# Performance work log

Measured on AMD Instinct MI355X. Metric: run time of the kernel, lower is better.

## Reference

```python
import jax, jax.numpy as jnp
import numpy as np

B, S, D, H = 2, 2048, 1024, 16
HD = D // H

def setup_inputs() -> dict:
    key = jax.random.key(0)
    ks = jax.random.split(key, 9)
    s = 1.0 / np.sqrt(D)
    return {
        "x": jax.random.normal(ks[0], (B, S, D), jnp.float32),
        "Wq": jax.random.normal(ks[1], (D, D), jnp.float32) * s,
        "bq": jnp.zeros((D,), jnp.float32),
        "Wk": jax.random.normal(ks[2], (D, D), jnp.float32) * s,
        "bk": jnp.zeros((D,), jnp.float32),
        "Wv": jax.random.normal(ks[3], (D, D), jnp.float32) * s,
        "bv": jnp.zeros((D,), jnp.float32),
        "Wo": jax.random.normal(ks[4], (D, D), jnp.float32) * s,
        "bo": jnp.zeros((D,), jnp.float32),
    }

def reference(x, Wq, bq, Wk, bk, Wv, bv, Wo, bo):
    b, s, d = x.shape
    def split_heads(t):
        return t.reshape(b, s, H, HD).transpose(0, 2, 1, 3)  # [B,H,S,HD]
    q = split_heads(x @ Wq + bq)
    k = split_heads(x @ Wk + bk)
    v = split_heads(x @ Wv + bv)
    scores = jnp.einsum('bhqd,bhkd->bhqk', q, k) / jnp.sqrt(jnp.float32(HD))
    causal = jnp.tril(jnp.ones((s, s), bool))  # True = keep
    scores = jnp.where(causal, scores, -jnp.inf)
    attn = jax.nn.softmax(scores, axis=-1)
    out = jnp.einsum('bhqk,bhkd->bhqd', attn, v)  # [B,H,S,HD]
    out = out.transpose(0, 2, 1, 3).reshape(b, s, d)
    return out @ Wo + bo
```

## Files before the change

### kernel.cpp

```cpp
#include <hip/hip_runtime.h>

typedef unsigned short u16;
typedef unsigned int u32;
typedef __attribute__((ext_vector_type(8))) short bf16x8;
typedef __attribute__((ext_vector_type(4))) float f32x4;

#define BB 2
#define SS 2048
#define DD 1024
#define HH 16
#define HD 64
#define MM (BB * SS)

__device__ inline float u2f(u32 u) { return __uint_as_float(u); }
__device__ inline u16 f2bf(float f) {
  u32 u = __float_as_uint(f);
  return (u16)((u + 0x7fffu + ((u >> 16) & 1u)) >> 16);
}

__device__ inline int sw(int r, int ci) { return r * 64 + (((ci ^ (r & 7)) & 7) << 3); }

typedef const __attribute__((address_space(1))) void* gas_ptr;
typedef __attribute__((address_space(3))) void* las_ptr;
__device__ __forceinline__ void gll16(const void* g, void* l) {
  __builtin_amdgcn_global_load_lds((gas_ptr)g, (las_ptr)l, 16, 0, 0);
}

__global__ __launch_bounds__(256) void prep(const float* __restrict__ x, u16* __restrict__ xb,
                                            const float* __restrict__ W0, const float* __restrict__ W1,
                                            const float* __restrict__ W2, const float* __restrict__ W3,
                                            u16* __restrict__ Wt) {
  int z = blockIdx.z;
  int t = threadIdx.x;
  if (z >= 4) {
    int gid = (z - 4) * 256 + blockIdx.y * 16 + blockIdx.x;
    int i = (gid * 256 + t) * 8;
    float4 a = *(const float4*)(x + i);
    float4 b = *(const float4*)(x + i + 4);
    uint4 o;
    o.x = (u32)f2bf(a.x) | ((u32)f2bf(a.y) << 16);
    o.y = (u32)f2bf(a.z) | ((u32)f2bf(a.w) << 16);
    o.z = (u32)f2bf(b.x) | ((u32)f2bf(b.y) << 16);
    o.w = (u32)f2bf(b.z) | ((u32)f2bf(b.w) << 16);
    *(uint4*)(xb + i) = o;
    return;
  }
  const float* W = (z == 0) ? W0 : (z == 1) ? W1 : (z == 2) ? W2 : W3;
  u16* out = Wt + (size_t)z * (DD * DD);
  __shared__ __align__(16) u16 T[64][72];
  int n0 = blockIdx.x * 64, k0 = blockIdx.y * 64;
#pragma unroll
  for (int p = 0; p < 4; ++p) {
    int kr = (t >> 4) + p * 16;
    int c4 = (t & 15) * 4;
    float4 v = *(const float4*)&W[(size_t)(k0 + kr) * DD + n0 + c4];
    T[c4 + 0][kr] = f2bf(v.x);
    T[c4 + 1][kr] = f2bf(v.y);
    T[c4 + 2][kr] = f2bf(v.z);
    T[c4 + 3][kr] = f2bf(v.w);
  }
  __syncthreads();
#pragma unroll
  for (int p = 0; p < 2; ++p) {
    int n = (t >> 3) + p * 32;
    int c8 = (t & 7) * 8;
    uint4 v = *(const uint4*)&T[n][c8];
    *(uint4*)&out[(size_t)(n0 + n) * DD + k0 + c8] = v;
  }
}

__global__ __launch_bounds__(256, 3) void gemm_qkv(const u16* __restrict__ xb, const u16* __restrict__ Wt,
                                                   const float* __restrict__ bq, const float* __restrict__ bk,
                                                   const float* __restrict__ bv,
                                                   u16* __restrict__ Qb, u16* __restrict__ Kb, u16* __restrict__ Vtb) {
  __shared__ __align__(16) u16 As[2][128 * 32];
  __shared__ __align__(16) u16 Bs[2][128 * 32];
  const int tid = threadIdx.x, lane = tid & 63, wv = tid >> 6;
  const int wm = (wv >> 1) * 64, wn = (wv & 1) * 64;
  const int l16 = lane & 15, quad = lane >> 4;

  const int id = blockIdx.x;
  const int xcd = id & 7, inner = id >> 3;
  const int mg = xcd >> 1, ng = xcd & 1;
  const int im = inner & 7, rest = inner >> 3;
  const int in_ = rest & 3, z = rest >> 2;
  const int m0 = (mg * 8 + im) * 128, n0 = (ng * 4 + in_) * 128;

  const u16* Bt = Wt + (size_t)z * (DD * DD);
  const float* bias = (z == 0) ? bq : (z == 1) ? bk : bv;

  const int r0 = tid >> 2, k8 = (tid & 3) << 3;
  const u16* Ap0 = &xb[(size_t)(m0 + r0) * DD + k8];
  const u16* Ap1 = Ap0 + (size_t)64 * DD;
  const u16* Bp0 = &Bt[(size_t)(n0 + r0) * DD + k8];
  const u16* Bp1 = Bp0 + (size_t)64 * DD;

  gll16(Ap0, &As[0][wv * 512]);
  gll16(Ap1, &As[0][2048 + wv * 512]);
  gll16(Bp0, &Bs[0][wv * 512]);
  gll16(Bp1, &Bs[0][2048 + wv * 512]);

  f32x4 acc[4][4];
  f32x4 zero = {0.f, 0.f, 0.f, 0.f};
#pragma unroll
  for (int i = 0; i < 4; ++i)
#pragma unroll
    for (int j = 0; j < 4; ++j) acc[i][j] = zero;

  __syncthreads();

  for (int kk = 0; kk < 32; ++kk) {
    const int cur = kk & 1;
    if (kk + 1 < 32) {
      const int nxt = cur ^ 1;
      const int ko = (kk + 1) * 32;
      gll16(Ap0 + ko, &As[nxt][wv * 512]);
      gll16(Ap1 + ko, &As[nxt][2048 + wv * 512]);
      gll16(Bp0 + ko, &Bs[nxt][wv * 512]);
      gll16(Bp1 + ko, &Bs[nxt][2048 + wv * 512]);
    }
    bf16x8 af[4], bg[4];
#pragma unroll
    for (int i = 0; i < 4; ++i) {
      af[i] = *(const bf16x8*)&As[cur][(wm + i * 16 + l16) * 32 + quad * 8];
      bg[i] = *(const bf16x8*)&Bs[cur][(wn + i * 16 + l16) * 32 + quad * 8];
    }
#pragma unroll
    for (int i = 0; i < 4; ++i)
#pragma unroll
      for (int j = 0; j < 4; ++j)
        acc[i][j] = __builtin_amdgcn_mfma_f32_16x16x32_bf16(af[i], bg[j], acc[i][j], 0, 0, 0);
    __syncthreads();
  }

  const float qsc = (z == 0) ? 0.180336880f : 1.0f;
  if (z == 2) {
#pragma unroll
    for (int i = 0; i < 4; ++i) {
#pragma unroll
      for (int j = 0; j < 4; ++j) {
        int col = n0 + wn + j * 16 + l16;
        float bcol = bias[col];
        int hh = col >> 6, dd = col & 63;
        int row0 = m0 + wm + i * 16 + quad * 4;
        int bb = row0 >> 11, s0 = row0 & (SS - 1);
        int sbase = (s0 & ~63) + 16 * quad + ((s0 >> 4) & 3);
        size_t base = (((size_t)((bb * HH + hh) * HD + dd)) << 11) + sbase;
#pragma unroll
        for (int r = 0; r < 4; ++r)
          Vtb[base + 4 * r] = f2bf(acc[i][j][r] + bcol);
      }
    }
  } else {
    u16* out = (z == 0) ? Qb : Kb;
#pragma unroll
    for (int i = 0; i < 4; ++i) {
#pragma unroll
      for (int j = 0; j < 4; ++j) {
        int col = n0 + wn + j * 16 + l16;
        float bcol = bias[col];
        int hh = col >> 6, dd = col & 63;
#pragma unroll
        for (int r = 0; r < 4; ++r) {
          int row = m0 + wm + i * 16 + quad * 4 + r;
          int bb = row >> 11, s = row & (SS - 1);
          out[((size_t)((bb * HH + hh) * SS + s) << 6) | dd] = f2bf((acc[i][j][r] + bcol) * qsc);
        }
      }
    }
  }
}

__global__ __launch_bounds__(256, 3) void gemm_out(const u16* __restrict__ Ub, const u16* __restrict__ Wot,
                                                   const float* __restrict__ bo, float* __restrict__ out) {
  __shared__ __align__(16) u16 As[2][128 * 32];
  __shared__ __align__(16) u16 Bs[2][64 * 32];
  const int tid = threadIdx.x, lane = tid & 63, wv = tid >> 6;
  const int wm = (wv >> 1) * 64, wn = (wv & 1) * 32;
  const int l16 = lane & 15, quad = lane >> 4;
  const int r0 = tid >> 2, k8 = (tid & 3) << 3;

  const int id = blockIdx.x;
  const int xcd = id & 7, inner = id >> 3;
  const int mg = xcd >> 1, ng = xcd & 1;
  const int im = inner & 7, in_ = inner >> 3;
  const int m0 = (mg * 8 + im) * 128, n0 = (ng * 8 + in_) * 64;

  const u16* Ap0 = &Ub[(size_t)(m0 + r0) * DD + k8];
  const u16* Ap1 = Ap0 + (size_t)64 * DD;
  const u16* Bp0 = &Wot[(size_t)(n0 + r0) * DD + k8];

  gll16(Ap0, &As[0][wv * 512]);
  gll16(Ap1, &As[0][2048 + wv * 512]);
  gll16(Bp0, &Bs[0][wv * 512]);

  f32x4 acc[4][2];
  f32x4 zero = {0.f, 0.f, 0.f, 0.f};
#pragma unroll
  for (int i = 0; i < 4; ++i) { acc[i][0] = zero; acc[i][1] = zero; }

  __syncthreads();

  for (int kk = 0; kk < 32; ++kk) {
    const int cur = kk & 1;
    if (kk + 1 < 32) {
      const int nxt = cur ^ 1;
      const int ko = (kk + 1) * 32;
      gll16(Ap0 + ko, &As[nxt][wv * 512]);
      gll16(Ap1 + ko, &As[nxt][2048 + wv * 512]);
      gll16(Bp0 + ko, &Bs[nxt][wv * 512]);
    }
    bf16x8 af[4], bg[2];
#pragma unroll
    for (int i = 0; i < 4; ++i) af[i] = *(const bf16x8*)&As[cur][(wm + i * 16 + l16) * 32 + quad * 8];
#pragma unroll
    for (int j = 0; j < 2; ++j) bg[j] = *(const bf16x8*)&Bs[cur][(wn + j * 16 + l16) * 32 + quad * 8];
#pragma unroll
    for (int i = 0; i < 4; ++i)
#pragma unroll
      for (int j = 0; j < 2; ++j)
        acc[i][j] = __builtin_amdgcn_mfma_f32_16x16x32_bf16(af[i], bg[j], acc[i][j], 0, 0, 0);
    __syncthreads();
  }

#pragma unroll
  for (int i = 0; i < 4; ++i) {
#pragma unroll
    for (int j = 0; j < 2; ++j) {
      int col = n0 + wn + j * 16 + l16;
      float bcol = bo[col];
#pragma unroll
      for (int r = 0; r < 4; ++r) {
        int row = m0 + wm + i * 16 + quad * 4 + r;
        out[(size_t)row * DD + col] = acc[i][j][r] + bcol;
      }
    }
  }
}

__global__ __launch_bounds__(256, 2) void attention_mfma(const u16* __restrict__ Q, const u16* __restrict__ K,
                                                         const u16* __restrict__ Vt, u16* __restrict__ Uo) {
  const int tid = threadIdx.x, lane = tid & 63, wv = tid >> 6;
  const int l16 = lane & 15, quad = lane >> 4;
  const int bh = blockIdx.x & 31;
  const int b = bh >> 4, h = bh & 15;
  const int gq = blockIdx.x >> 5;
  const int qA = (gq < 8) ? gq : 23 - gq;
  const int qB = 31 - qA;
  const int q0A = qA * 64, q0B = qB * 64;
  const u16* Qh = Q + (size_t)(b * HH + h) * SS * HD;
  const u16* Kh = K + (size_t)(b * HH + h) * SS * HD;
  const u16* Vh = Vt + (size_t)(b * HH + h) * HD * SS;

  __shared__ __align__(16) u16 K_lds[2][64 * 64];
  __shared__ __align__(16) u16 V_lds[2][64 * 64];
  __shared__ __align__(16) u16 p_lds[2][64][72];

  bf16x8 qfA0, qfA1, qfB0, qfB1;
  {
    const u16* qa = &Qh[(size_t)(q0A + wv * 16 + l16) * HD + quad * 8];
    qfA0 = *(const bf16x8*)qa;
    qfA1 = *(const bf16x8*)(qa + 32);
    const u16* qb = &Qh[(size_t)(q0B + wv * 16 + l16) * HD + quad * 8];
    qfB0 = *(const bf16x8*)qb;
    qfB1 = *(const bf16x8*)(qb + 32);
  }

  f32x4 zero = {0.f, 0.f, 0.f, 0.f};
  f32x4 oA[4], oB[4];
#pragma unroll
  for (int j = 0; j < 4; ++j) { oA[j] = zero; oB[j] = zero; }
  float lA[4] = {0.f, 0.f, 0.f, 0.f}, lB[4] = {0.f, 0.f, 0.f, 0.f};

  const int sr = tid >> 2, ci = tid & 3, cc = ci << 3;
  const u16* Kg = &Kh[(size_t)sr * HD + cc];
  const u16* Vg = &Vh[(size_t)sr * SS + cc];
  const int ktiles = qB + 1;
  const int wlo = sw(sr, ci), whi = sw(sr, ci + 4);

  uint4 ka = *(const uint4*)Kg, kb = *(const uint4*)(Kg + 32);
  uint4 va = *(const uint4*)Vg, vb = *(const uint4*)(Vg + 32);
  *(uint4*)&K_lds[0][wlo] = ka;
  *(uint4*)&K_lds[0][whi] = kb;
  *(uint4*)&V_lds[0][wlo] = va;
  *(uint4*)&V_lds[0][whi] = vb;
  {
    const u16* Kn = Kg + (size_t)64 * HD;
    const u16* Vn = Vg + 64;
    ka = *(const uint4*)Kn; kb = *(const uint4*)(Kn + 32);
    va = *(const uint4*)Vn; vb = *(const uint4*)(Vn + 32);
  }
  __syncthreads();

  for (int t = 0; t < ktiles; ++t) {
    const int cur = t & 1;
    const bool doA = (t <= qA);

    f32x4 sA[4], sB[4];
#pragma unroll
    for (int n = 0; n < 4; ++n) {
      const int kr = n * 16 + l16;
      bf16x8 kf0 = *(const bf16x8*)&K_lds[cur][sw(kr, quad)];
      bf16x8 kf1 = *(const bf16x8*)&K_lds[cur][sw(kr, quad + 4)];
      f32x4 aB = zero;
      aB = __builtin_amdgcn_mfma_f32_16x16x32_bf16(qfB0, kf0, aB, 0, 0, 0);
      aB = __builtin_amdgcn_mfma_f32_16x16x32_bf16(qfB1, kf1, aB, 0, 0, 0);
      sB[n] = aB;
      if (doA) {
        f32x4 aA = zero;
        aA = __builtin_amdgcn_mfma_f32_16x16x32_bf16(qfA0, kf0, aA, 0, 0, 0);
        aA = __builtin_amdgcn_mfma_f32_16x16x32_bf16(qfA1, kf1, aA, 0, 0, 0);
        sA[n] = aA;
      }
    }

    {
      const int rel = q0B + wv * 16 + quad * 4 - t * 64;
#pragma unroll
      for (int rr = 0; rr < 4; ++rr) {
        float p0 = __builtin_amdgcn_exp2f(sB[0][rr]);
        float p1 = __builtin_amdgcn_exp2f(sB[1][rr]);
        float p2 = __builtin_amdgcn_exp2f(sB[2][rr]);
        float p3 = __builtin_amdgcn_exp2f(sB[3][rr]);
        if (t == qB) {
          int row = rel + rr;
          p0 = (l16 <= row) ? p0 : 0.f;
          p1 = (16 + l16 <= row) ? p1 : 0.f;
          p2 = (32 + l16 <= row) ? p2 : 0.f;
          p3 = (48 + l16 <= row) ? p3 : 0.f;
        }
        lB[rr] += (p0 + p1) + (p2 + p3);
        uint2 pk;
        pk.x = (__float_as_uint(p0) >> 16) | (__float_as_uint(p1) & 0xffff0000u);
        pk.y = (__float_as_uint(p2) >> 16) | (__float_as_uint(p3) & 0xffff0000u);
        *(uint2*)&p_lds[1][wv * 16 + quad * 4 + rr][l16 * 4] = pk;
      }
    }
    if (doA) {
      const int rel = q0A + wv * 16 + quad * 4 - t * 64;
#pragma unroll
      for (int rr = 0; rr < 4; ++rr) {
        float p0 = __builtin_amdgcn_exp2f(sA[0][rr]);
        float p1 = __builtin_amdgcn_exp2f(sA[1][rr]);
        float p2 = __builtin_amdgcn_exp2f(sA[2][rr]);
        float p3 = __builtin_amdgcn_exp2f(sA[3][rr]);
        if (t == qA) {
          int row = rel + rr;
          p0 = (l16 <= row) ? p0 : 0.f;
          p1 = (16 + l16 <= row) ? p1 : 0.f;
          p2 = (32 + l16 <= row) ? p2 : 0.f;
          p3 = (48 + l16 <= row) ? p3 : 0.f;
        }
        lA[rr] += (p0 + p1) + (p2 + p3);
        uint2 pk;
        pk.x = (__float_as_uint(p0) >> 16) | (__float_as_uint(p1) & 0xffff0000u);
        pk.y = (__float_as_uint(p2) >> 16) | (__float_as_uint(p3) & 0xffff0000u);
        *(uint2*)&p_lds[0][wv * 16 + quad * 4 + rr][l16 * 4] = pk;
      }
    }

    if (doA) {
      bf16x8 pB0 = *(const bf16x8*)&p_lds[1][wv * 16 + l16][quad * 8];
      bf16x8 pB1 = *(const bf16x8*)&p_lds[1][wv * 16 + l16][32 + quad * 8];
      bf16x8 pA0 = *(const bf16x8*)&p_lds[0][wv * 16 + l16][quad * 8];
      bf16x8 pA1 = *(const bf16x8*)&p_lds[0][wv * 16 + l16][32 + quad * 8];
#pragma unroll
      for (int j = 0; j < 4; ++j) {
        const int vr = j * 16 + l16;
        bf16x8 vf0 = *(const bf16x8*)&V_lds[cur][sw(vr, quad)];
        bf16x8 vf1 = *(const bf16x8*)&V_lds[cur][sw(vr, quad + 4)];
        oB[j] = __builtin_amdgcn_mfma_f32_16x16x32_bf16(pB0, vf0, oB[j], 0, 0, 0);
        oB[j] = __builtin_amdgcn_mfma_f32_16x16x32_bf16(pB1, vf1, oB[j], 0, 0, 0);
        oA[j] = __builtin_amdgcn_mfma_f32_16x16x32_bf16(pA0, vf0, oA[j], 0, 0, 0);
        oA[j] = __builtin_amdgcn_mfma_f32_16x16x32_bf16(pA1, vf1, oA[j], 0, 0, 0);
      }
    } else {
      bf16x8 pB0 = *(const bf16x8*)&p_lds[1][wv * 16 + l16][quad * 8];
      bf16x8 pB1 = *(const bf16x8*)&p_lds[1][wv * 16 + l16][32 + quad * 8];
#pragma unroll
      for (int j = 0; j < 4; ++j) {
        const int vr = j * 16 + l16;
        bf16x8 vf0 = *(const bf16x8*)&V_lds[cur][sw(vr, quad)];
        bf16x8 vf1 = *(const bf16x8*)&V_lds[cur][sw(vr, quad + 4)];
        oB[j] = __builtin_amdgcn_mfma_f32_16x16x32_bf16(pB0, vf0, oB[j], 0, 0, 0);
        oB[j] = __builtin_amdgcn_mfma_f32_16x16x32_bf16(pB1, vf1, oB[j], 0, 0, 0);
      }
    }

    if (t + 1 < ktiles) {
      const int nxt = cur ^ 1;
      *(uint4*)&K_lds[nxt][wlo] = ka;
      *(uint4*)&K_lds[nxt][whi] = kb;
      *(uint4*)&V_lds[nxt][wlo] = va;
      *(uint4*)&V_lds[nxt][whi] = vb;
      if (t + 2 < ktiles) {
        const u16* Kn = Kg + (size_t)(t + 2) * 64 * HD;
        const u16* Vn = Vg + (t + 2) * 64;
        ka = *(const uint4*)Kn; kb = *(const uint4*)(Kn + 32);
        va = *(const uint4*)Vn; vb = *(const uint4*)(Vn + 32);
      }
    }
    __syncthreads();
  }

#pragma unroll
  for (int rr = 0; rr < 4; ++rr) {
    float a = lA[rr], c = lB[rr];
#pragma unroll
    for (int off = 1; off < 16; off <<= 1) {
      a += __shfl_xor(a, off);
      c += __shfl_xor(c, off);
    }
    lA[rr] = 1.0f / a;
    lB[rr] = 1.0f / c;
  }

#pragma unroll
  for (int j = 0; j < 4; ++j) {
#pragma unroll
    for (int r = 0; r < 4; ++r) {
      int rowA = q0A + wv * 16 + quad * 4 + r;
      int rowB = q0B + wv * 16 + quad * 4 + r;
      Uo[(size_t)(b * SS + rowA) * DD + (h << 6) + j * 16 + l16] = f2bf(oA[j][r] * lA[r]);
      Uo[(size_t)(b * SS + rowB) * DD + (h << 6) + j * 16 + l16] = f2bf(oB[j][r] * lB[r]);
    }
  }
}

extern "C" void kernel_launch(void* const* d_in, const int* in_sizes, int n_in,
                              void* d_out, int out_size, void* d_ws, size_t ws_size,
                              hipStream_t stream) {
  const float* x  = (const float*)d_in[0];
  const float* Wq = (const float*)d_in[1];
  const float* bq = (const float*)d_in[2];
  const float* Wk = (const float*)d_in[3];
  const float* bk = (const float*)d_in[4];
  const float* Wv = (const float*)d_in[5];
  const float* bv = (const float*)d_in[6];
  const float* Wo = (const float*)d_in[7];
  const float* bo = (const float*)d_in[8];
  float* out = (float*)d_out;

  char* ws = (char*)d_ws;
  u16* xb  = (u16*)(ws);
  u16* Wt  = (u16*)(ws + ((size_t)8 << 20));
  u16* Qb  = (u16*)(ws + ((size_t)16 << 20));
  u16* Kb  = (u16*)(ws + ((size_t)24 << 20));
  u16* Vtb = (u16*)(ws + ((size_t)32 << 20));
  u16* Ub  = (u16*)(ws + ((size_t)40 << 20));

  prep<<<dim3(16, 16, 12), dim3(256), 0, stream>>>(x, xb, Wq, Wk, Wv, Wo, Wt);
  gemm_qkv<<<dim3(768), dim3(256), 0, stream>>>(xb, Wt, bq, bk, bv, Qb, Kb, Vtb);
  attention_mfma<<<dim3(512), dim3(256), 0, stream>>>(Qb, Kb, Vtb, Ub);
  gemm_out<<<dim3(512), dim3(256), 0, stream>>>(Ub, Wt + (size_t)3 * DD * DD, bo, out);
}
```

Before: 173.2 us.

## Compute transposed scores to keep P in registers, drop P LDS round-trip

Attention now computes S^T = K·Q^T with MFMA so each lane's exp'd probabilities land directly in the A-operand layout for the P·V MFMA, removing the p_lds shared-memory write/read. The paired A/B query tiles per block are replaced by one query tile per block, launched heaviest-first with 1024 blocks, and launch bounds are raised to allow 4 blocks per CU. The V-transpose store in the QKV GEMM is changed to a permuted key order so four bf16 values go out as one 8-byte store, matching the new P register layout. The trade-off is that each block loads the K/V tiles for only one query tile instead of two, so global and LDS traffic per unit of work roughly doubles, and causal load balance now relies on scheduling order rather than pairing.

```diff
diff --git a/kernel.cpp b/kernel.cpp
--- a/kernel.cpp
+++ b/kernel.cpp
@@ -24,6 +24,10 @@
 typedef __attribute__((address_space(3))) void* las_ptr;
 __device__ __forceinline__ void gll16(const void* g, void* l) {
   __builtin_amdgcn_global_load_lds((gas_ptr)g, (las_ptr)l, 16, 0, 0);
+}
+
+__device__ __forceinline__ u32 pk2(float a, float b) {
+  return (__float_as_uint(a) >> 16) | (__float_as_uint(b) & 0xffff0000u);
 }
 
 __global__ __launch_bounds__(256) void prep(const float* __restrict__ x, u16* __restrict__ xb,
@@ -142,13 +146,14 @@
         int col = n0 + wn + j * 16 + l16;
         float bcol = bias[col];
         int hh = col >> 6, dd = col & 63;
-        int row0 = m0 + wm + i * 16 + quad * 4;
+        int row0 = m0 + wm + i * 16;
         int bb = row0 >> 11, s0 = row0 & (SS - 1);
-        int sbase = (s0 & ~63) + 16 * quad + ((s0 >> 4) & 3);
+        int sbase = (s0 & ~63) + (i >> 1) * 32 + quad * 8 + (i & 1) * 4;
         size_t base = (((size_t)((bb * HH + hh) * HD + dd)) << 11) + sbase;
-#pragma unroll
-        for (int r = 0; r < 4; ++r)
-          Vtb[base + 4 * r] = f2bf(acc[i][j][r] + bcol);
+        uint2 pv;
+        pv.x = (u32)f2bf(acc[i][j][0] + bcol) | ((u32)f2bf(acc[i][j][1] + bcol) << 16);
+        pv.y = (u32)f2bf(acc[i][j][2] + bcol) | ((u32)f2bf(acc[i][j][3] + bcol) << 16);
+        *(uint2*)&Vtb[base] = pv;
       }
     }
   } else {
@@ -238,44 +243,38 @@
   }
 }
 
-__global__ __launch_bounds__(256, 2) void attention_mfma(const u16* __restrict__ Q, const u16* __restrict__ K,
+__global__ __launch_bounds__(256, 4) void attention_mfma(const u16* __restrict__ Q, const u16* __restrict__ K,
                                                          const u16* __restrict__ Vt, u16* __restrict__ Uo) {
   const int tid = threadIdx.x, lane = tid & 63, wv = tid >> 6;
   const int l16 = lane & 15, quad = lane >> 4;
   const int bh = blockIdx.x & 31;
   const int b = bh >> 4, h = bh & 15;
-  const int gq = blockIdx.x >> 5;
-  const int qA = (gq < 8) ? gq : 23 - gq;
-  const int qB = 31 - qA;
-  const int q0A = qA * 64, q0B = qB * 64;
+  const int qt = 31 - (blockIdx.x >> 5);
+  const int q0 = qt * 64;
   const u16* Qh = Q + (size_t)(b * HH + h) * SS * HD;
   const u16* Kh = K + (size_t)(b * HH + h) * SS * HD;
   const u16* Vh = Vt + (size_t)(b * HH + h) * HD * SS;
 
   __shared__ __align__(16) u16 K_lds[2][64 * 64];
   __shared__ __align__(16) u16 V_lds[2][64 * 64];
-  __shared__ __align__(16) u16 p_lds[2][64][72];
-
-  bf16x8 qfA0, qfA1, qfB0, qfB1;
+
+  bf16x8 qf0, qf1;
   {
-    const u16* qa = &Qh[(size_t)(q0A + wv * 16 + l16) * HD + quad * 8];
-    qfA0 = *(const bf16x8*)qa;
-    qfA1 = *(const bf16x8*)(qa + 32);
-    const u16* qb = &Qh[(size_t)(q0B + wv * 16 + l16) * HD + quad * 8];
-    qfB0 = *(const bf16x8*)qb;
-    qfB1 = *(const bf16x8*)(qb + 32);
+    const u16* qp = &Qh[(size_t)(q0 + wv * 16 + l16) * HD + quad * 8];
+    qf0 = *(const bf16x8*)qp;
+    qf1 = *(const bf16x8*)(qp + 32);
   }
 
   f32x4 zero = {0.f, 0.f, 0.f, 0.f};
-  f32x4 oA[4], oB[4];
-#pragma unroll
-  for (int j = 0; j < 4; ++j) { oA[j] = zero; oB[j] = zero; }
-  float lA[4] = {0.f, 0.f, 0.f, 0.f}, lB[4] = {0.f, 0.f, 0.f, 0.f};
+  f32x4 o[4];
+#pragma unroll
+  for (int j = 0; j < 4; ++j) o[j] = zero;
+  float lsum = 0.f;
 
   const int sr = tid >> 2, ci = tid & 3, cc = ci << 3;
   const u16* Kg = &Kh[(size_t)sr * HD + cc];
   const u16* Vg = &Vh[(size_t)sr * SS + cc];
-  const int ktiles = qB + 1;
+  const int ktiles = qt + 1;
   const int wlo = sw(sr, ci), whi = sw(sr, ci + 4);
 
   uint4 ka = *(const uint4*)Kg, kb = *(const uint4*)(Kg + 32);
@@ -294,97 +293,52 @@
 
   for (int t = 0; t < ktiles; ++t) {
     const int cur = t & 1;
-    const bool doA = (t <= qA);
-
-    f32x4 sA[4], sB[4];
+
+    f32x4 sT[4];
 #pragma unroll
     for (int n = 0; n < 4; ++n) {
       const int kr = n * 16 + l16;
       bf16x8 kf0 = *(const bf16x8*)&K_lds[cur][sw(kr, quad)];
       bf16x8 kf1 = *(const bf16x8*)&K_lds[cur][sw(kr, quad + 4)];
-      f32x4 aB = zero;
-      aB = __builtin_amdgcn_mfma_f32_16x16x32_bf16(qfB0, kf0, aB, 0, 0, 0);
-      aB = __builtin_amdgcn_mfma_f32_16x16x32_bf16(qfB1, kf1, aB, 0, 0, 0);
-      sB[n] = aB;
-      if (doA) {
-        f32x4 aA = zero;
-        aA = __builtin_amdgcn_mfma_f32_16x16x32_bf16(qfA0, kf0, aA, 0, 0, 0);
-        aA = __builtin_amdgcn_mfma_f32_16x16x32_bf16(qfA1, kf1, aA, 0, 0, 0);
-        sA[n] = aA;
-      }
-    }
-
-    {
-      const int rel = q0B + wv * 16 + quad * 4 - t * 64;
-#pragma unroll
-      for (int rr = 0; rr < 4; ++rr) {
-        float p0 = __builtin_amdgcn_exp2f(sB[0][rr]);
-        float p1 = __builtin_amdgcn_exp2f(sB[1][rr]);
-        float p2 = __builtin_amdgcn_exp2f(sB[2][rr]);
-        float p3 = __builtin_amdgcn_exp2f(sB[3][rr]);
-        if (t == qB) {
-          int row = rel + rr;
-          p0 = (l16 <= row) ? p0 : 0.f;
-          p1 = (16 + l16 <= row) ? p1 : 0.f;
-          p2 = (32 + l16 <= row) ? p2 : 0.f;
-          p3 = (48 + l16 <= row) ? p3 : 0.f;
-        }
-        lB[rr] += (p0 + p1) + (p2 + p3);
-        uint2 pk;
-        pk.x = (__float_as_uint(p0) >> 16) | (__float_as_uint(p1) & 0xffff0000u);
-        pk.y = (__float_as_uint(p2) >> 16) | (__float_as_uint(p3) & 0xffff0000u);
-        *(uint2*)&p_lds[1][wv * 16 + quad * 4 + rr][l16 * 4] = pk;
-      }
-    }
-    if (doA) {
-      const int rel = q0A + wv * 16 + quad * 4 - t * 64;
-#pragma unroll
-      for (int rr = 0; rr < 4; ++rr) {
-        float p0 = __builtin_amdgcn_exp2f(sA[0][rr]);
-        float p1 = __builtin_amdgcn_exp2f(sA[1][rr]);
-        float p2 = __builtin_amdgcn_exp2f(sA[2][rr]);
-        float p3 = __builtin_amdgcn_exp2f(sA[3][rr]);
-        if (t == qA) {
-          int row = rel + rr;
-          p0 = (l16 <= row) ? p0 : 0.f;
-          p1 = (16 + l16 <= row) ? p1 : 0.f;
-          p2 = (32 + l16 <= row) ? p2 : 0.f;
-          p3 = (48 + l16 <= row) ? p3 : 0.f;
-        }
-        lA[rr] += (p0 + p1) + (p2 + p3);
-        uint2 pk;
-        pk.x = (__float_as_uint(p0) >> 16) | (__float_as_uint(p1) & 0xffff0000u);
-        pk.y = (__float_as_uint(p2) >> 16) | (__float_as_uint(p3) & 0xffff0000u);
-        *(uint2*)&p_lds[0][wv * 16 + quad * 4 + rr][l16 * 4] = pk;
-      }
-    }
-
-    if (doA) {
-      bf16x8 pB0 = *(const bf16x8*)&p_lds[1][wv * 16 + l16][quad * 8];
-      bf16x8 pB1 = *(const bf16x8*)&p_lds[1][wv * 16 + l16][32 + quad * 8];
-      bf16x8 pA0 = *(const bf16x8*)&p_lds[0][wv * 16 + l16][quad * 8];
-      bf16x8 pA1 = *(const bf16x8*)&p_lds[0][wv * 16 + l16][32 + quad * 8];
-#pragma unroll
-      for (int j = 0; j < 4; ++j) {
-        const int vr = j * 16 + l16;
-        bf16x8 vf0 = *(const bf16x8*)&V_lds[cur][sw(vr, quad)];
-        bf16x8 vf1 = *(const bf16x8*)&V_lds[cur][sw(vr, quad + 4)];
-        oB[j] = __builtin_amdgcn_mfma_f32_16x16x32_bf16(pB0, vf0, oB[j], 0, 0, 0);
-        oB[j] = __builtin_amdgcn_mfma_f32_16x16x32_bf16(pB1, vf1, oB[j], 0, 0, 0);
-        oA[j] = __builtin_amdgcn_mfma_f32_16x16x32_bf16(pA0, vf0, oA[j], 0, 0, 0);
-        oA[j] = __builtin_amdgcn_mfma_f32_16x16x32_bf16(pA1, vf1, oA[j], 0, 0, 0);
-      }
-    } else {
-      bf16x8 pB0 = *(const bf16x8*)&p_lds[1][wv * 16 + l16][quad * 8];
-      bf16x8 pB1 = *(const bf16x8*)&p_lds[1][wv * 16 + l16][32 + quad * 8];
-#pragma unroll
-      for (int j = 0; j < 4; ++j) {
-        const int vr = j * 16 + l16;
-        bf16x8 vf0 = *(const bf16x8*)&V_lds[cur][sw(vr, quad)];
-        bf16x8 vf1 = *(const bf16x8*)&V_lds[cur][sw(vr, quad + 4)];
-        oB[j] = __builtin_amdgcn_mfma_f32_16x16x32_bf16(pB0, vf0, oB[j], 0, 0, 0);
-        oB[j] = __builtin_amdgcn_mfma_f32_16x16x32_bf16(pB1, vf1, oB[j], 0, 0, 0);
-      }
+      f32x4 a = zero;
+      a = __builtin_amdgcn_mfma_f32_16x16x32_bf16(kf0, qf0, a, 0, 0, 0);
+      a = __builtin_amdgcn_mfma_f32_16x16x32_bf16(kf1, qf1, a, 0, 0, 0);
+      sT[n] = a;
+    }
+
+    float p[4][4];
+#pragma unroll
+    for (int n = 0; n < 4; ++n)
+#pragma unroll
+      for (int r = 0; r < 4; ++r) p[n][r] = __builtin_amdgcn_exp2f(sT[n][r]);
+    if (t == qt) {
+      const int qloc = wv * 16 + l16;
+#pragma unroll
+      for (int n = 0; n < 4; ++n)
+#pragma unroll
+        for (int r = 0; r < 4; ++r)
+          if (n * 16 + quad * 4 + r > qloc) p[n][r] = 0.f;
+    }
+#pragma unroll
+    for (int n = 0; n < 4; ++n) lsum += (p[n][0] + p[n][1]) + (p[n][2] + p[n][3]);
+
+    union { uint4 u; bf16x8 v; } pa0, pa1;
+    pa0.u.x = pk2(p[0][0], p[0][1]);
+    pa0.u.y = pk2(p[0][2], p[0][3]);
+    pa0.u.z = pk2(p[1][0], p[1][1]);
+    pa0.u.w = pk2(p[1][2], p[1][3]);
+    pa1.u.x = pk2(p[2][0], p[2][1]);
+    pa1.u.y = pk2(p[2][2], p[2][3]);
+    pa1.u.z = pk2(p[3][0], p[3][1]);
+    pa1.u.w = pk2(p[3][2], p[3][3]);
+
+#pragma unroll
+    for (int j = 0; j < 4; ++j) {
+      const int vr = j * 16 + l16;
+      bf16x8 vf0 = *(const bf16x8*)&V_lds[cur][sw(vr, quad)];
+      bf16x8 vf1 = *(const bf16x8*)&V_lds[cur][sw(vr, quad + 4)];
+      o[j] = __builtin_amdgcn_mfma_f32_16x16x32_bf16(pa0.v, vf0, o[j], 0, 0, 0);
+      o[j] = __builtin_amdgcn_mfma_f32_16x16x32_bf16(pa1.v, vf1, o[j], 0, 0, 0);
     }
 
     if (t + 1 < ktiles) {
@@ -403,26 +357,18 @@
     __syncthreads();
   }
 
-#pragma unroll
-  for (int rr = 0; rr < 4; ++rr) {
-    float a = lA[rr], c = lB[rr];
-#pragma unroll
-    for (int off = 1; off < 16; off <<= 1) {
-      a += __shfl_xor(a, off);
-      c += __shfl_xor(c, off);
-    }
-    lA[rr] = 1.0f / a;
-    lB[rr] = 1.0f / c;
-  }
+  lsum += __shfl_xor(lsum, 16);
+  lsum += __shfl_xor(lsum, 32);
+  float linv[4];
+#pragma unroll
+  for (int r = 0; r < 4; ++r) linv[r] = 1.0f / __shfl(lsum, quad * 4 + r);
 
 #pragma unroll
   for (int j = 0; j < 4; ++j) {
 #pragma unroll
     for (int r = 0; r < 4; ++r) {
-      int rowA = q0A + wv * 16 + quad * 4 + r;
-      int rowB = q0B + wv * 16 + quad * 4 + r;
-      Uo[(size_t)(b * SS + rowA) * DD + (h << 6) + j * 16 + l16] = f2bf(oA[j][r] * lA[r]);
-      Uo[(size_t)(b * SS + rowB) * DD + (h << 6) + j * 16 + l16] = f2bf(oB[j][r] * lB[r]);
+      int row = q0 + wv * 16 + quad * 4 + r;
+      Uo[(size_t)(b * SS + row) * DD + (h << 6) + j * 16 + l16] = f2bf(o[j][r] * linv[r]);
     }
   }
 }
@@ -451,6 +397,6 @@
 
   prep<<<dim3(16, 16, 12), dim3(256), 0, stream>>>(x, xb, Wq, Wk, Wv, Wo, Wt);
   gemm_qkv<<<dim3(768), dim3(256), 0, stream>>>(xb, Wt, bq, bk, bv, Qb, Kb, Vtb);
-  attention_mfma<<<dim3(512), dim3(256), 0, stream>>>(Qb, Kb, Vtb, Ub);
+  attention_mfma<<<dim3(1024), dim3(256), 0, stream>>>(Qb, Kb, Vtb, Ub);
   gemm_out<<<dim3(512), dim3(256), 0, stream>>>(Ub, Wt + (size_t)3 * DD * DD, bo, out);
 }
```

Result: no change. 173.6 us (+0.3%).
